# Kernel tuning notes

Hardware: AMD Instinct MI355X
Metric: run time of the kernel (lower is better)

Reference implementation:

```python
import jax, jax.numpy as jnp
import numpy as np

STRIDE, PAD, DIL = 1, 1, 1


def setup_inputs() -> dict:
    key = jax.random.key(0)
    k1, k2, k3, k4, k5 = jax.random.split(key, 5)
    N, Cin, H, W = 8, 256, 64, 64
    Cout, K = 256, 3
    x = jax.random.normal(k1, (N, Cin, H, W), dtype=jnp.float32)
    offset = jax.random.normal(k2, (N, 2 * K * K, H, W), dtype=jnp.float32)
    mask = jax.random.uniform(k3, (N, K * K, H, W), dtype=jnp.float32)
    weight = jax.random.normal(k4, (Cout, Cin, K, K), dtype=jnp.float32) * 0.02
    bias = jax.random.normal(k5, (Cout,), dtype=jnp.float32)
    return {"x": x, "offset": offset, "mask": mask, "weight": weight, "bias": bias}


def _gather(im_flat, idx):
    # im_flat: (N, Goff, Cg, H*W); idx: (N, Goff, KK, Ho, Wo) int32
    # -> (N, Goff, Cg, KK, Ho, Wo)
    f = lambda imf, ix: imf[:, ix]
    return jax.vmap(jax.vmap(f))(im_flat, idx)


def _deform_conv2d(x, offset, mask, weight, bias):
    N, Cin, H, W = x.shape
    Cout, Cin_g, Kh, Kw = weight.shape
    KK = Kh * Kw
    Goff = offset.shape[1] // (2 * KK)
    Ho = (H + 2 * PAD - (DIL * (Kh - 1) + 1)) // STRIDE + 1
    Wo = (W + 2 * PAD - (DIL * (Kw - 1) + 1)) // STRIDE + 1

    # base sampling grid per kernel tap: (KK, Ho, Wo)
    py = (jnp.arange(Kh)[:, None] * DIL + jnp.arange(Ho)[None, :] * STRIDE - PAD).astype(jnp.float32)
    px = (jnp.arange(Kw)[:, None] * DIL + jnp.arange(Wo)[None, :] * STRIDE - PAD).astype(jnp.float32)
    y_base = jnp.broadcast_to(py[:, None, :, None], (Kh, Kw, Ho, Wo)).reshape(KK, Ho, Wo)
    x_base = jnp.broadcast_to(px[None, :, None, :], (Kh, Kw, Ho, Wo)).reshape(KK, Ho, Wo)

    off = offset.reshape(N, Goff, KK, 2, Ho, Wo)  # [...,0]=dy, [...,1]=dx
    ys = y_base[None, None] + off[:, :, :, 0]  # (N, Goff, KK, Ho, Wo)
    xs = x_base[None, None] + off[:, :, :, 1]

    Cg = Cin // Goff
    im_flat = x.reshape(N, Goff, Cg, H * W)

    y0 = jnp.floor(ys)
    x0 = jnp.floor(xs)
    acc = jnp.zeros((N, Goff, Cg, KK, Ho, Wo), dtype=x.dtype)
    for dy in (0.0, 1.0):
        for dx in (0.0, 1.0):
            yi = y0 + dy
            xi = x0 + dx
            wgt = (1.0 - jnp.abs(ys - yi)) * (1.0 - jnp.abs(xs - xi))
            valid = (yi >= 0) & (yi < H) & (xi >= 0) & (xi < W)
            idx = (jnp.clip(yi, 0, H - 1) * W + jnp.clip(xi, 0, W - 1)).astype(jnp.int32)
            g = _gather(im_flat, idx)  # (N,Goff,Cg,KK,Ho,Wo)
            acc = acc + g * (wgt * valid.astype(x.dtype))[:, :, None]

    m = mask.reshape(N, Goff, KK, Ho, Wo)
    sampled = acc * m[:, :, None]  # DCNv2 modulation

    # grouped conv accumulate as GEMM over (Cin_g*KK)
    gw = Cin // Cin_g
    cols = sampled.reshape(N, gw, Cin_g * KK, Ho * Wo)
    wflat = weight.reshape(gw, Cout // gw, Cin_g * KK)
    out = jnp.einsum('goc,ngcl->ngol', wflat, cols).reshape(N, Cout, Ho, Wo)
    return out + bias[None, :, None, None]


def reference(x, offset, mask, weight, bias):
    return _deform_conv2d(x, offset, mask, weight, bias)
```

## Files before the change

### kernel.cpp

```cpp
#include <hip/hip_runtime.h>
#include <stdint.h>

typedef unsigned int u32;
typedef unsigned short u16;
typedef float f32x4 __attribute__((ext_vector_type(4)));
typedef __fp16 h16x2 __attribute__((ext_vector_type(2)));
typedef _Float16 f16x8 __attribute__((ext_vector_type(8)));
typedef float f4u __attribute__((ext_vector_type(4), aligned(4)));

#define NB   8
#define CIN  256
#define HH   64
#define WW   64
#define HW   4096
#define COUT 256
#define NPX  128
#define BSTR 264

__device__ __forceinline__ u32 pkh(float lo, float hi) {
  h16x2 h = __builtin_amdgcn_cvt_pkrtz(lo, hi);
  return __builtin_bit_cast(u32, h);
}
union HU { u32 u; h16x2 h; };

__global__ __launch_bounds__(256) void prep_all(const float* __restrict__ x,
                                                const float* __restrict__ wgt,
                                                u32* __restrict__ xT,
                                                u32* __restrict__ W2f32) {
  int b = blockIdx.x;
  int t = threadIdx.x;
  if (b < 2048) {
    __shared__ __align__(16) u32 tile[16][132];
    int n = b >> 8, hw0 = (b & 255) << 4;
    int hwq = (t & 3) << 2;
    int cp0 = t >> 2;
    const float* xb = x + (size_t)n * CIN * HW + hw0 + hwq;
#pragma unroll
    for (int it = 0; it < 2; ++it) {
      int cp = (it << 6) + cp0;
      int c = cp << 1;
      f4u v0 = *(const f4u*)(xb + (size_t)c * HW);
      f4u v1 = *(const f4u*)(xb + (size_t)(c + 1) * HW);
      tile[hwq + 0][cp] = pkh(v0.x, v1.x);
      tile[hwq + 1][cp] = pkh(v0.y, v1.y);
      tile[hwq + 2][cp] = pkh(v0.z, v1.z);
      tile[hwq + 3][cp] = pkh(v0.w, v1.w);
    }
    __syncthreads();
    u32* outp = xT + ((size_t)(n * HW + hw0)) * 128;
    int cq = t & 31, hb = t >> 5;
#pragma unroll
    for (int it = 0; it < 2; ++it) {
      int hwl = (it << 3) + hb;
      uint4 v = *(const uint4*)&tile[hwl][cq << 2];
      *(uint4*)(outp + (size_t)hwl * 128 + (cq << 2)) = v;
    }
  } else {
    int tt = (b - 2048) * 256 + t;
    int cp = tt & 127, co = tt >> 7;
    int c = cp << 1;
    const float* p = wgt + ((size_t)co * CIN + c) * 9;
    f4u q0 = *(const f4u*)(p + 0);
    f4u q1 = *(const f4u*)(p + 4);
    f4u q2 = *(const f4u*)(p + 8);
    f4u q3 = *(const f4u*)(p + 12);
    float e16 = p[16], e17 = p[17];
    float a0[9], a1[9];
    a0[0]=q0.x; a0[1]=q0.y; a0[2]=q0.z; a0[3]=q0.w;
    a0[4]=q1.x; a0[5]=q1.y; a0[6]=q1.z; a0[7]=q1.w; a0[8]=q2.x;
    a1[0]=q2.y; a1[1]=q2.z; a1[2]=q2.w;
    a1[3]=q3.x; a1[4]=q3.y; a1[5]=q3.z; a1[6]=q3.w; a1[7]=e16; a1[8]=e17;
    int cc = c >> 5;
    int j = (c >> 1) & 3;
    int lane = (co & 15) | (((c >> 3) & 3) << 4);
    int tile_ = ((co >> 6) << 2) | ((co >> 4) & 3);
#pragma unroll
    for (int kk = 0; kk < 9; ++kk) {
      int frag = (kk * 8 + cc) * 16 + tile_;
      W2f32[(size_t)frag * 256 + lane * 4 + j] = pkh(a0[kk], a1[kk]);
    }
  }
}

__global__ __launch_bounds__(1024, 4) void dcn_main(
    const float* __restrict__ offset, const float* __restrict__ mask,
    const float* __restrict__ bias, const u16* __restrict__ xT,
    const u16* __restrict__ W2f, float* __restrict__ out) {
  __shared__ __align__(16) u16 Bs[2][NPX * BSTR];
  __shared__ __align__(8)  uint2 swl[1152];
  __shared__ __align__(8)  ushort4 sol[1152];

  int bid = blockIdx.x;
  int n = bid & 7;
  int hp = bid >> 3;
  int t = threadIdx.x;
  int lane = t & 63;
  int w = t >> 6;
  bool prod = (w >= 8);

  for (int i = t; i < 1152; i += 1024) {
    int kk = i >> 7, p = i & 127;
    int ky = kk / 3, kx = kk - ky * 3;
    int sp = (hp << 7) + p;
    int ho = (hp << 1) + (p >> 6);
    float dy = offset[(((size_t)n * 18 + kk * 2 + 0) << 12) + sp];
    float dx = offset[(((size_t)n * 18 + kk * 2 + 1) << 12) + sp];
    float m  = mask  [(((size_t)n * 9  + kk) << 12) + sp];
    float ys = (float)(ky + ho - 1) + dy;
    float xs = (float)(kx + (p & 63) - 1) + dx;
    float y0f = floorf(ys), x0f = floorf(xs);
    float fy = ys - y0f, fx = xs - x0f;
    int y0 = (int)y0f, x0 = (int)x0f;
    int y1 = y0 + 1, x1 = x0 + 1;
    float vy0 = (y0 >= 0 && y0 < HH) ? 1.f : 0.f;
    float vy1 = (y1 >= 0 && y1 < HH) ? 1.f : 0.f;
    float vx0 = (x0 >= 0 && x0 < WW) ? 1.f : 0.f;
    float vx1 = (x1 >= 0 && x1 < WW) ? 1.f : 0.f;
    float w0 = (1.f - fy) * (1.f - fx) * m * vy0 * vx0;
    float w1 = (1.f - fy) * fx * m * vy0 * vx1;
    float w2 = fy * (1.f - fx) * m * vy1 * vx0;
    float w3 = fy * fx * m * vy1 * vx1;
    int iy0 = min(max(y0, 0), HH - 1), iy1 = min(max(y1, 0), HH - 1);
    int ix0 = min(max(x0, 0), WW - 1), ix1 = min(max(x1, 0), WW - 1);
    ushort4 pv;
    pv.x = (u16)((iy0 << 6) + ix0);
    pv.y = (u16)((iy0 << 6) + ix1);
    pv.z = (u16)((iy1 << 6) + ix0);
    pv.w = (u16)((iy1 << 6) + ix1);
    swl[i] = make_uint2(pkh(w0, w1), pkh(w2, w3));
    sol[i] = pv;
  }
  __syncthreads();

  f32x4 acc[2][8];
#pragma unroll
  for (int a = 0; a < 2; ++a)
#pragma unroll
    for (int b2 = 0; b2 < 8; ++b2) acc[a][b2] = {0.f, 0.f, 0.f, 0.f};

  const char* xTn = (const char*)xT + ((size_t)n * HW << 9);
  int ml = lane & 15, q = lane >> 4;
  int hw32 = t >> 5;
  int l32 = t & 31;
  int strip = w & 7;
  int tile0 = ((strip >> 1) << 2) + ((strip & 1) << 1);
  const char* bch = xTn + (l32 << 4);
  int tp = t - 512;
  int ch = tp & 31;
  int ph = tp >> 5;
  const char* bchp = xTn + (ch << 4);

#define CMB(G, WT) do {                                                \
    float wt = (WT);                                                   \
    HU h0, h1, h2, h3;                                                 \
    h0.u = (G).x; h1.u = (G).y; h2.u = (G).z; h3.u = (G).w;            \
    s0 = __builtin_fmaf((float)h0.h.x, wt, s0);                        \
    s1 = __builtin_fmaf((float)h0.h.y, wt, s1);                        \
    s2 = __builtin_fmaf((float)h1.h.x, wt, s2);                        \
    s3 = __builtin_fmaf((float)h1.h.y, wt, s3);                        \
    s4 = __builtin_fmaf((float)h2.h.x, wt, s4);                        \
    s5 = __builtin_fmaf((float)h2.h.y, wt, s5);                        \
    s6 = __builtin_fmaf((float)h3.h.x, wt, s6);                        \
    s7 = __builtin_fmaf((float)h3.h.y, wt, s7);                        \
  } while (0)

  auto build0 = [&](int g) {
    int px = (g << 5) + hw32;
    uint2 wu = swl[px];
    ushort4 pv = sol[px];
    HU ha, hb; ha.u = wu.x; hb.u = wu.y;
    uint4 G0 = *(const uint4*)(bch + ((int)pv.x << 9));
    uint4 G1 = *(const uint4*)(bch + ((int)pv.y << 9));
    uint4 G2 = *(const uint4*)(bch + ((int)pv.z << 9));
    uint4 G3 = *(const uint4*)(bch + ((int)pv.w << 9));
    float s0=0.f,s1=0.f,s2=0.f,s3=0.f,s4=0.f,s5=0.f,s6=0.f,s7=0.f;
    CMB(G0, (float)ha.h.x);
    CMB(G1, (float)ha.h.y);
    CMB(G2, (float)hb.h.x);
    CMB(G3, (float)hb.h.y);
    uint4 pkd;
    pkd.x = pkh(s0, s1); pkd.y = pkh(s2, s3);
    pkd.z = pkh(s4, s5); pkd.w = pkh(s6, s7);
    *(uint4*)((char*)&Bs[0][0] + px * (BSTR * 2) + (l32 << 4)) = pkd;
  };

  auto af_load = [&](int fidx, int mt) {
    return *(const f16x8*)(W2f + (((size_t)((fidx << 4) + tile0 + mt)) << 9) +
                           (lane << 3));
  };

#pragma unroll
  for (int g = 0; g < 4; ++g) build0(g);

  f16x8 ca, cb;
  if (!prod) { ca = af_load(0, 0); cb = af_load(0, 1); }
  __syncthreads();

#pragma unroll 1
  for (int kk = 0; kk < 9; ++kk) {
    if (prod) {
      if (kk < 8) {
        char* Bw = (char*)&Bs[(kk & 1) ^ 1][0];
        int base = (kk + 1) << 7;
        uint2 wA = swl[base + ph];
        ushort4 pvA = sol[base + ph];
        uint4 A0 = *(const uint4*)(bchp + ((int)pvA.x << 9));
        uint4 A1 = *(const uint4*)(bchp + ((int)pvA.y << 9));
        uint4 A2 = *(const uint4*)(bchp + ((int)pvA.z << 9));
        uint4 A3 = *(const uint4*)(bchp + ((int)pvA.w << 9));
#pragma unroll
        for (int s = 0; s < 8; ++s) {
          uint4 B0, B1, B2, B3; uint2 wB;
          if (s < 7) {
            ushort4 pv = sol[base + ((s + 1) << 4) + ph];
            wB = swl[base + ((s + 1) << 4) + ph];
            B0 = *(const uint4*)(bchp + ((int)pv.x << 9));
            B1 = *(const uint4*)(bchp + ((int)pv.y << 9));
            B2 = *(const uint4*)(bchp + ((int)pv.z << 9));
            B3 = *(const uint4*)(bchp + ((int)pv.w << 9));
          }
          {
            HU ha, hb; ha.u = wA.x; hb.u = wA.y;
            float s0=0.f,s1=0.f,s2=0.f,s3=0.f,s4=0.f,s5=0.f,s6=0.f,s7=0.f;
            CMB(A0, (float)ha.h.x);
            CMB(A1, (float)ha.h.y);
            CMB(A2, (float)hb.h.x);
            CMB(A3, (float)hb.h.y);
            uint4 pkd;
            pkd.x = pkh(s0, s1); pkd.y = pkh(s2, s3);
            pkd.z = pkh(s4, s5); pkd.w = pkh(s6, s7);
            *(uint4*)(Bw + ((s << 4) + ph) * (BSTR * 2) + (ch << 4)) = pkd;
          }
          wA = wB; A0 = B0; A1 = B1; A2 = B2; A3 = B3;
        }
      }
    } else {
      const char* Br = (const char*)&Bs[kk & 1][0];
      int fbase = kk << 3;
#pragma unroll
      for (int cc = 0; cc < 8; ++cc) {
        f16x8 na, nb;
        if (cc < 7) {
          na = af_load(fbase + cc + 1, 0);
          nb = af_load(fbase + cc + 1, 1);
        } else if (kk < 8) {
          na = af_load(fbase + 8, 0);
          nb = af_load(fbase + 8, 1);
        }
        __builtin_amdgcn_s_setprio(1);
#pragma unroll
        for (int nt = 0; nt < 8; ++nt) {
          f16x8 b = *(const f16x8*)(Br + ((nt << 4) + ml) * (BSTR * 2) +
                                    (cc << 6) + (q << 4));
          acc[0][nt] = __builtin_amdgcn_mfma_f32_16x16x32_f16(ca, b, acc[0][nt], 0, 0, 0);
          acc[1][nt] = __builtin_amdgcn_mfma_f32_16x16x32_f16(cb, b, acc[1][nt], 0, 0, 0);
        }
        __builtin_amdgcn_s_setprio(0);
        ca = na; cb = nb;
      }
    }
    __syncthreads();
  }

  if (!prod) {
    size_t ob = (size_t)n * COUT * HW + ((size_t)hp << 7);
#pragma unroll
    for (int mt = 0; mt < 2; ++mt) {
#pragma unroll
      for (int r = 0; r < 4; ++r) {
        int co = (strip << 5) + (mt << 4) + (q << 2) + r;
        float bv = bias[co];
#pragma unroll
        for (int nt = 0; nt < 8; ++nt) {
          int px = (nt << 4) + ml;
          out[ob + (size_t)co * HW + px] = acc[mt][nt][r] + bv;
        }
      }
    }
  }
}

extern "C" void kernel_launch(void* const* d_in, const int* in_sizes, int n_in,
                              void* d_out, int out_size, void* d_ws, size_t ws_size,
                              hipStream_t stream) {
  const float* x      = (const float*)d_in[0];
  const float* offset = (const float*)d_in[1];
  const float* mask   = (const float*)d_in[2];
  const float* weight = (const float*)d_in[3];
  const float* bias   = (const float*)d_in[4];
  float* out = (float*)d_out;

  u16* xT  = (u16*)d_ws;
  u16* W2f = (u16*)((char*)d_ws + (size_t)NB * HW * CIN * 2);

  prep_all<<<2176, 256, 0, stream>>>(x, weight, (u32*)xT, (u32*)W2f);
  dcn_main<<<256, 1024, 0, stream>>>(offset, mask, bias, xT, W2f, out);
}
```

Before: 150.6 us.

## Shrink producer warps to 4 and software-pipeline LDS B-fragment loads for MFMA

The block drops from 1024 to 768 threads, so 4 producer wavefronts now gather two pixels per step, which doubles the number of in-flight global gathers per thread. The initial build loop is rewritten as a strided loop over all threads. Consumer wavefronts prefetch the next chunk's eight B fragments from LDS into registers while the current MFMAs run. The aim is more memory-level parallelism per producer and hiding LDS latency behind the MFMAs. The cost is higher register pressure and half as many producer threads.

```diff
diff --git a/kernel.cpp b/kernel.cpp
--- a/kernel.cpp
+++ b/kernel.cpp
@@ -82,7 +82,7 @@
   }
 }
 
-__global__ __launch_bounds__(1024, 4) void dcn_main(
+__global__ __launch_bounds__(768, 3) void dcn_main(
     const float* __restrict__ offset, const float* __restrict__ mask,
     const float* __restrict__ bias, const u16* __restrict__ xT,
     const u16* __restrict__ W2f, float* __restrict__ out) {
@@ -98,7 +98,7 @@
   int w = t >> 6;
   bool prod = (w >= 8);
 
-  for (int i = t; i < 1152; i += 1024) {
+  for (int i = t; i < 1152; i += 768) {
     int kk = i >> 7, p = i & 127;
     int ky = kk / 3, kx = kk - ky * 3;
     int sp = (hp << 7) + p;
@@ -140,15 +140,12 @@
 
   const char* xTn = (const char*)xT + ((size_t)n * HW << 9);
   int ml = lane & 15, q = lane >> 4;
-  int hw32 = t >> 5;
-  int l32 = t & 31;
   int strip = w & 7;
   int tile0 = ((strip >> 1) << 2) + ((strip & 1) << 1);
-  const char* bch = xTn + (l32 << 4);
   int tp = t - 512;
   int ch = tp & 31;
   int ph = tp >> 5;
-  const char* bchp = xTn + (ch << 4);
+  const char* bchp = xTn + ((t & 31) << 4);
 
 #define CMB(G, WT) do {                                                \
     float wt = (WT);                                                   \
@@ -164,15 +161,21 @@
     s7 = __builtin_fmaf((float)h3.h.y, wt, s7);                        \
   } while (0)
 
-  auto build0 = [&](int g) {
-    int px = (g << 5) + hw32;
+  auto af_load = [&](int fidx, int mt) {
+    return *(const f16x8*)(W2f + (((size_t)((fidx << 4) + tile0 + mt)) << 9) +
+                           (lane << 3));
+  };
+
+  for (int i = t; i < 4096; i += 768) {
+    int px = i >> 5, cch = i & 31;
+    const char* bc = xTn + (cch << 4);
     uint2 wu = swl[px];
     ushort4 pv = sol[px];
     HU ha, hb; ha.u = wu.x; hb.u = wu.y;
-    uint4 G0 = *(const uint4*)(bch + ((int)pv.x << 9));
-    uint4 G1 = *(const uint4*)(bch + ((int)pv.y << 9));
-    uint4 G2 = *(const uint4*)(bch + ((int)pv.z << 9));
-    uint4 G3 = *(const uint4*)(bch + ((int)pv.w << 9));
+    uint4 G0 = *(const uint4*)(bc + ((int)pv.x << 9));
+    uint4 G1 = *(const uint4*)(bc + ((int)pv.y << 9));
+    uint4 G2 = *(const uint4*)(bc + ((int)pv.z << 9));
+    uint4 G3 = *(const uint4*)(bc + ((int)pv.w << 9));
     float s0=0.f,s1=0.f,s2=0.f,s3=0.f,s4=0.f,s5=0.f,s6=0.f,s7=0.f;
     CMB(G0, (float)ha.h.x);
     CMB(G1, (float)ha.h.y);
@@ -181,16 +184,8 @@
     uint4 pkd;
     pkd.x = pkh(s0, s1); pkd.y = pkh(s2, s3);
     pkd.z = pkh(s4, s5); pkd.w = pkh(s6, s7);
-    *(uint4*)((char*)&Bs[0][0] + px * (BSTR * 2) + (l32 << 4)) = pkd;
-  };
-
-  auto af_load = [&](int fidx, int mt) {
-    return *(const f16x8*)(W2f + (((size_t)((fidx << 4) + tile0 + mt)) << 9) +
-                           (lane << 3));
-  };
-
-#pragma unroll
-  for (int g = 0; g < 4; ++g) build0(g);
+    *(uint4*)((char*)&Bs[0][0] + px * (BSTR * 2) + (cch << 4)) = pkd;
+  }
 
   f16x8 ca, cb;
   if (!prod) { ca = af_load(0, 0); cb = af_load(0, 1); }
@@ -208,18 +203,32 @@
         uint4 A1 = *(const uint4*)(bchp + ((int)pvA.y << 9));
         uint4 A2 = *(const uint4*)(bchp + ((int)pvA.z << 9));
         uint4 A3 = *(const uint4*)(bchp + ((int)pvA.w << 9));
-#pragma unroll
-        for (int s = 0; s < 8; ++s) {
-          uint4 B0, B1, B2, B3; uint2 wB;
-          if (s < 7) {
-            ushort4 pv = sol[base + ((s + 1) << 4) + ph];
-            wB = swl[base + ((s + 1) << 4) + ph];
-            B0 = *(const uint4*)(bchp + ((int)pv.x << 9));
-            B1 = *(const uint4*)(bchp + ((int)pv.y << 9));
-            B2 = *(const uint4*)(bchp + ((int)pv.z << 9));
-            B3 = *(const uint4*)(bchp + ((int)pv.w << 9));
+        uint2 wB = swl[base + 8 + ph];
+        ushort4 pvB = sol[base + 8 + ph];
+        uint4 B0 = *(const uint4*)(bchp + ((int)pvB.x << 9));
+        uint4 B1 = *(const uint4*)(bchp + ((int)pvB.y << 9));
+        uint4 B2 = *(const uint4*)(bchp + ((int)pvB.z << 9));
+        uint4 B3 = *(const uint4*)(bchp + ((int)pvB.w << 9));
+#pragma unroll
+        for (int pr2 = 0; pr2 < 8; ++pr2) {
+          uint4 C0, C1, C2, C3, D0, D1, D2, D3; uint2 wC, wD;
+          if (pr2 < 7) {
+            int nb = base + ((pr2 + 1) << 4);
+            ushort4 pvC = sol[nb + ph];
+            wC = swl[nb + ph];
+            C0 = *(const uint4*)(bchp + ((int)pvC.x << 9));
+            C1 = *(const uint4*)(bchp + ((int)pvC.y << 9));
+            C2 = *(const uint4*)(bchp + ((int)pvC.z << 9));
+            C3 = *(const uint4*)(bchp + ((int)pvC.w << 9));
+            ushort4 pvD = sol[nb + 8 + ph];
+            wD = swl[nb + 8 + ph];
+            D0 = *(const uint4*)(bchp + ((int)pvD.x << 9));
+            D1 = *(const uint4*)(bchp + ((int)pvD.y << 9));
+            D2 = *(const uint4*)(bchp + ((int)pvD.z << 9));
+            D3 = *(const uint4*)(bchp + ((int)pvD.w << 9));
           }
           {
+            int px = (pr2 << 4) + ph;
             HU ha, hb; ha.u = wA.x; hb.u = wA.y;
             float s0=0.f,s1=0.f,s2=0.f,s3=0.f,s4=0.f,s5=0.f,s6=0.f,s7=0.f;
             CMB(A0, (float)ha.h.x);
@@ -229,34 +238,60 @@
             uint4 pkd;
             pkd.x = pkh(s0, s1); pkd.y = pkh(s2, s3);
             pkd.z = pkh(s4, s5); pkd.w = pkh(s6, s7);
-            *(uint4*)(Bw + ((s << 4) + ph) * (BSTR * 2) + (ch << 4)) = pkd;
+            *(uint4*)(Bw + px * (BSTR * 2) + (ch << 4)) = pkd;
           }
-          wA = wB; A0 = B0; A1 = B1; A2 = B2; A3 = B3;
+          {
+            int px = (pr2 << 4) + 8 + ph;
+            HU ha, hb; ha.u = wB.x; hb.u = wB.y;
+            float s0=0.f,s1=0.f,s2=0.f,s3=0.f,s4=0.f,s5=0.f,s6=0.f,s7=0.f;
+            CMB(B0, (float)ha.h.x);
+            CMB(B1, (float)ha.h.y);
+            CMB(B2, (float)hb.h.x);
+            CMB(B3, (float)hb.h.y);
+            uint4 pkd;
+            pkd.x = pkh(s0, s1); pkd.y = pkh(s2, s3);
+            pkd.z = pkh(s4, s5); pkd.w = pkh(s6, s7);
+            *(uint4*)(Bw + px * (BSTR * 2) + (ch << 4)) = pkd;
+          }
+          wA = wC; A0 = C0; A1 = C1; A2 = C2; A3 = C3;
+          wB = wD; B0 = D0; B1 = D1; B2 = D2; B3 = D3;
         }
       }
     } else {
       const char* Br = (const char*)&Bs[kk & 1][0];
       int fbase = kk << 3;
+      f16x8 bb[8], nn[8];
+#pragma unroll
+      for (int nt = 0; nt < 8; ++nt)
+        bb[nt] = *(const f16x8*)(Br + ((nt << 4) + ml) * (BSTR * 2) + (q << 4));
 #pragma unroll
       for (int cc = 0; cc < 8; ++cc) {
-        f16x8 na, nb;
+        f16x8 ca2, cb2;
         if (cc < 7) {
-          na = af_load(fbase + cc + 1, 0);
-          nb = af_load(fbase + cc + 1, 1);
+#pragma unroll
+          for (int nt = 0; nt < 8; ++nt)
+            nn[nt] = *(const f16x8*)(Br + ((nt << 4) + ml) * (BSTR * 2) +
+                                     ((cc + 1) << 6) + (q << 4));
+          ca2 = af_load(fbase + cc + 1, 0);
+          cb2 = af_load(fbase + cc + 1, 1);
         } else if (kk < 8) {
-          na = af_load(fbase + 8, 0);
-          nb = af_load(fbase + 8, 1);
+          ca2 = af_load(fbase + 8, 0);
+          cb2 = af_load(fbase + 8, 1);
         }
         __builtin_amdgcn_s_setprio(1);
 #pragma unroll
         for (int nt = 0; nt < 8; ++nt) {
-          f16x8 b = *(const f16x8*)(Br + ((nt << 4) + ml) * (BSTR * 2) +
-                                    (cc << 6) + (q << 4));
-          acc[0][nt] = __builtin_amdgcn_mfma_f32_16x16x32_f16(ca, b, acc[0][nt], 0, 0, 0);
-          acc[1][nt] = __builtin_amdgcn_mfma_f32_16x16x32_f16(cb, b, acc[1][nt], 0, 0, 0);
+          acc[0][nt] = __builtin_amdgcn_mfma_f32_16x16x32_f16(ca, bb[nt], acc[0][nt], 0, 0, 0);
+          acc[1][nt] = __builtin_amdgcn_mfma_f32_16x16x32_f16(cb, bb[nt], acc[1][nt], 0, 0, 0);
         }
         __builtin_amdgcn_s_setprio(0);
-        ca = na; cb = nb;
+        if (cc < 7) {
+#pragma unroll
+          for (int nt = 0; nt < 8; ++nt) bb[nt] = nn[nt];
+          ca = ca2; cb = cb2;
+        } else if (kk < 8) {
+          ca = ca2; cb = cb2;
+        }
       }
     }
     __syncthreads();
@@ -294,5 +329,5 @@
   u16* W2f = (u16*)((char*)d_ws + (size_t)NB * HW * CIN * 2);
 
   prep_all<<<2176, 256, 0, stream>>>(x, weight, (u32*)xT, (u32*)W2f);
-  dcn_main<<<256, 1024, 0, stream>>>(offset, mask, bias, xT, W2f, out);
+  dcn_main<<<256, 768, 0, stream>>>(offset, mask, bias, xT, W2f, out);
 }
```

Measured after the change: 150.5 us. No clear change (-0.1%).
